# Kernel tuning notes

Hardware: AMD Instinct MI355X
Metric: run time of the kernel (lower is better)

The kernel has to match this reference:

```python
import jax, jax.numpy as jnp
import numpy as np

K = 7          # kernel_size (odd)
STRIDE = 1
PAD = K // 2
SIGMA_GUIDE = 1.0


def _unfold6(x, k, stride, pad):
    """torch F.unfold equivalent -> (bs, ch, k, k, oh, ow)."""
    bs, ch = x.shape[:2]
    patches = jax.lax.conv_general_dilated_patches(
        x, filter_shape=(k, k), window_strides=(stride, stride),
        padding=[(pad, pad), (pad, pad)])  # (bs, ch*k*k, oh, ow), channel-major
    oh, ow = patches.shape[2:]
    return patches.reshape(bs, ch, k, k, oh, ow)


def setup_inputs() -> dict:
    key = jax.random.key(0)
    k1, k2 = jax.random.split(key, 2)
    input = jax.random.normal(k1, (2, 32, 256, 256), dtype=jnp.float32)
    input_for_kernel = jax.random.normal(k2, (2, 3, 256, 256), dtype=jnp.float32)
    sigma_for_kernel = jnp.asarray(float(K) / 4.0, dtype=jnp.float32)  # Parameter init
    return {"input": input, "input_for_kernel": input_for_kernel,
            "sigma_for_kernel": sigma_for_kernel}


def reference(input, input_for_kernel, sigma_for_kernel):
    dt = input.dtype
    # spatial Gaussian kernel (truncated, normalized)
    r = jnp.arange(-(K // 2), K // 2 + 1, dtype=dt)
    g1 = jnp.exp(-0.5 * r * r / (sigma_for_kernel * sigma_for_kernel))
    g2 = g1[:, None] * g1[None, :]
    g2 = g2 / g2.sum()  # (K, K)

    # data-dependent range (guide) kernel: GaussKernel2dFn, channel_wise=False
    g = input_for_kernel / SIGMA_GUIDE                      # (b, cg, H, W)
    cols_g = _unfold6(g, K, STRIDE, PAD)                    # (b, cg, K, K, H, W)
    diff = cols_g - g[:, :, None, None]                     # center = window middle (stride 1)
    guide = jnp.exp(-0.5 * jnp.sum(diff * diff, axis=1, keepdims=True))  # (b,1,K,K,H,W)

    ker = g2[None, None, :, :, None, None] * guide          # (b,1,K,K,H,W)
    norm = ker.sum(axis=(2, 3), keepdims=True)
    ker = ker / (norm + (norm == 0).astype(dt))

    # ApplyKernelFn: unfold input, multiply by per-pixel kernel, sum over window
    in_cols = _unfold6(input, K, STRIDE, PAD)               # (b, c, K, K, H, W)
    out = jnp.einsum('bcklhw,bzklhw->bchw', in_cols, ker)
    return out
```

## Files before the change

### kernel.cpp

```cpp
#include <hip/hip_runtime.h>

#define KS    7
#define RAD   3
#define TW    32
#define TH    8
#define HR    14
#define PAIRS 21
#define NSITE (HR*2*PAIRS)
#define H     256
#define W     256
#define HWp   (H*W)
#define NTASK2 (HR*10*2)

typedef __fp16    h2raw __attribute__((ext_vector_type(2)));
typedef _Float16  f16x2 __attribute__((ext_vector_type(2)));

__device__ __forceinline__ unsigned pk(float a, float b) {
    h2raw h = __builtin_amdgcn_cvt_pkrtz(a, b);
    return __builtin_bit_cast(unsigned, h);
}
__device__ __forceinline__ f16x2 bch(unsigned u) {
    return __builtin_bit_cast(f16x2, u);
}

#if __has_builtin(__builtin_amdgcn_fdot2)
__device__ __forceinline__ float fdot2(f16x2 a, f16x2 b, float c) {
    return __builtin_amdgcn_fdot2(a, b, c, false);
}
#else
__device__ __forceinline__ float fdot2(f16x2 a, f16x2 b, float c) {
    return c + (float)a.x * (float)b.x + (float)a.y * (float)b.y;
}
#endif

#if __has_builtin(__builtin_amdgcn_exp2f)
__device__ __forceinline__ float fexp2(float x) { return __builtin_amdgcn_exp2f(x); }
#else
__device__ __forceinline__ float fexp2(float x) { return exp2f(x); }
#endif

__device__ __forceinline__ void pkfma(f16x2& d, f16x2 a, f16x2 b) {
    asm("v_pk_fma_f16 %0, %1, %2, %0" : "+v"(d) : "v"(a), "v"(b));
}

#define BAR() asm volatile("s_waitcnt lgkmcnt(0)\n\ts_barrier" ::: "memory")

#define ISSUE_IN(g) do {                                                    \
    _Pragma("unroll")                                                       \
    for (int j = 0; j < 2; ++j) {                                           \
        iA[j] = make_float4(0.f, 0.f, 0.f, 0.f);                            \
        iB[j] = iA[j]; iC[j] = iA[j]; iD[j] = iA[j];                        \
        if (tv[j]) {                                                        \
            const float* p = inb + (size_t)((g) * 8 + 4 * tcpp[j]) * HWp    \
                             + toff[j];                                     \
            iA[j] = *(const float4*)p;                                      \
            iB[j] = *(const float4*)(p + HWp);                              \
            iC[j] = *(const float4*)(p + 2 * HWp);                          \
            iD[j] = *(const float4*)(p + 3 * HWp);                          \
        }                                                                   \
    }                                                                       \
} while (0)

#define WRITE_IN(g) do {                                                    \
    _Pragma("unroll")                                                       \
    for (int j = 0; j < 2; ++j) {                                           \
        if (tok[j]) {                                                       \
            unsigned* bp = &dtu[(g)][ts0[j] * 4 + tcpp[j] * 2];             \
            *(uint2*)bp = make_uint2(pk(iA[j].y, iB[j].y),                  \
                                     pk(iC[j].y, iD[j].y));                 \
            *(uint2*)(bp + PAIRS * 4) = make_uint2(pk(iA[j].z, iB[j].z),    \
                                                   pk(iC[j].z, iD[j].z));   \
            if (!tq0[j])                                                    \
                *(uint2*)(bp + (PAIRS - 1) * 4) =                           \
                    make_uint2(pk(iA[j].x, iB[j].x), pk(iC[j].x, iD[j].x)); \
            if (!tq9[j])                                                    \
                *(uint2*)(bp + 4) =                                         \
                    make_uint2(pk(iA[j].w, iB[j].w), pk(iC[j].w, iD[j].w)); \
        }                                                                   \
    }                                                                       \
} while (0)

#define APPLY(g) do {                                                       \
    const uint4* dg = (const uint4*)&dtu[(g)][0];                           \
    float acc[8];                                                           \
    _Pragma("unroll") for (int c = 0; c < 8; ++c) acc[c] = 0.f;             \
    f16x2 A0 = (f16x2)0, A1 = (f16x2)0, A2 = (f16x2)0, A3 = (f16x2)0;       \
    _Pragma("unroll")                                                       \
    for (int i = 0; i < KS; ++i) {                                          \
        const int rb = (ty + i) * 2 * PAIRS;                                \
        uint4 rq[KS];                                                       \
        _Pragma("unroll")                                                   \
        for (int k = 0; k < KS; ++k) rq[k] = dg[rb + colAdd[k]];            \
        _Pragma("unroll")                                                   \
        for (int k = 0; k < KS; ++k) {                                      \
            f16x2 wh = bch(wkp[i * KS + k]);                                \
            pkfma(A0, wh, bch(rq[k].x));                                    \
            pkfma(A1, wh, bch(rq[k].y));                                    \
            pkfma(A2, wh, bch(rq[k].z));                                    \
            pkfma(A3, wh, bch(rq[k].w));                                    \
        }                                                                   \
        if (i == 3) {         \
            acc[0] += (float)A0.x; acc[1] += (float)A0.y;                   \
            acc[2] += (float)A1.x; acc[3] += (float)A1.y;                   \
            acc[4] += (float)A2.x; acc[5] += (float)A2.y;                   \
            acc[6] += (float)A3.x; acc[7] += (float)A3.y;                   \
            A0 = (f16x2)0; A1 = (f16x2)0; A2 = (f16x2)0; A3 = (f16x2)0;     \
        }                                                                   \
    }                                                                       \
    acc[0] += (float)A0.x; acc[1] += (float)A0.y;                           \
    acc[2] += (float)A1.x; acc[3] += (float)A1.y;                           \
    acc[4] += (float)A2.x; acc[5] += (float)A2.y;                           \
    acc[6] += (float)A3.x; acc[7] += (float)A3.y;                           \
    float* ob = out + ((size_t)b * 32 + (g) * 8) * HWp                      \
                + (size_t)Yo * W + Xo;                                      \
    _Pragma("unroll")                                                       \
    for (int c = 0; c < 8; ++c) ob[(size_t)c * HWp] = acc[c] * inv;         \
} while (0)

__global__ __launch_bounds__(256)
void bilateral_kernel(const float* __restrict__ in,
                      const float* __restrict__ guide,
                      const float* __restrict__ sigma_p,
                      float* __restrict__ out)
{
    __shared__ uint2 gt2[NSITE];
    __shared__ __align__(16) unsigned dtu[4][NSITE * 4];

    const int tid = threadIdx.x;
    const int tx  = tid & 31;
    const int ty  = tid >> 5;
    const int x0  = blockIdx.x * TW;
    const int y0  = blockIdx.y * TH;
    const int b   = blockIdx.z;

    const float* gb  = guide + (size_t)b * 3  * HWp;
    const float* inb = in    + (size_t)b * 32 * HWp;

    const float sigma = sigma_p[0];
    const float isig2 = 1.0f / (sigma * sigma);
    const float L2E   = 1.442695041f;
    const float SQL   = 1.201122409f;
    float lnT2[KS];
#pragma unroll
    for (int i = 0; i < KS; ++i) {
        float r = (float)(i - RAD);
        lnT2[i] = -0.5f * r * r * isig2 * L2E;
    }

    bool tok[2], tv[2], tq0[2], tq9[2];
    int  tcpp[2], toff[2], ts0[2];
#pragma unroll
    for (int j = 0; j < 2; ++j) {
        int t = tid + j * 256;
        tok[j] = t < NTASK2;
        int row = t / 20;
        int rem = t - row * 20;
        int q   = rem >> 1;
        tcpp[j] = rem & 1;
        int gy  = y0 - RAD + row;
        int gxb = x0 - 4 + 4 * q;
        tv[j]   = tok[j] && gy >= 0 && gy < H && gxb >= 0 && gxb < W;
        toff[j] = gy * W + gxb;
        ts0[j]  = row * 2 * PAIRS + 2 * q;
        tq0[j]  = (q == 0);
        tq9[j]  = (q == 9);
    }

    float4 gX = make_float4(0.f, 0.f, 0.f, 0.f), gY = gX, gZ = gX;
    int grow = 0, gq = 0;
    if (tid < HR * 10) {
        grow = tid / 10; gq = tid - grow * 10;
        int gy  = y0 - RAD + grow;
        int gxb = x0 - 4 + 4 * gq;
        if (gy >= 0 && gy < H && gxb >= 0 && gxb < W) {
            const float* p = gb + gy * W + gxb;
            gX = *(const float4*)p;
            gY = *(const float4*)(p + HWp);
            gZ = *(const float4*)(p + 2 * HWp);
        }
    }
    float4 iA[2], iB[2], iC[2], iD[2];
    ISSUE_IN(0);

    if (tid < HR * 10) {
        int s0 = grow * 2 * PAIRS + 2 * gq;
        const float xs[4] = {gX.x, gX.y, gX.z, gX.w};
        const float ys[4] = {gY.x, gY.y, gY.z, gY.w};
        const float zs[4] = {gZ.x, gZ.y, gZ.z, gZ.w};
        const int   st[4] = {s0 + PAIRS - 1, s0, s0 + PAIRS, s0 + 1};
#pragma unroll
        for (int j = 0; j < 4; ++j) {
            if ((gq == 0 && j == 0) || (gq == 9 && j == 3)) continue;
            float ax = xs[j] * SQL, ay = ys[j] * SQL, az = zs[j] * SQL;
            float qv = -0.5f * (ax * ax + ay * ay + az * az);
            gt2[st[j]] = make_uint2(pk(ax, ay), pk(az, qv));
        }
    }
    BAR();

    int colAdd[KS];
#pragma unroll
    for (int k = 0; k < KS; ++k) {
        int col = tx + k;
        colAdd[k] = (col & 1) * PAIRS + (col >> 1);
    }

    const int ccol = tx + RAD;
    uint2 cr = gt2[(ty + RAD) * 2 * PAIRS + (ccol & 1) * PAIRS + (ccol >> 1)];
    const f16x2 cxy = bch(cr.x);
    f16x2 czq = bch(cr.y);
    const float qc = (float)czq.y;
    f16x2 cz1;
    cz1.x = czq.x; cz1.y = (_Float16)1.0f;

    unsigned wkp[KS * KS];
    float nsum = 0.f;
#pragma unroll
    for (int i = 0; i < KS; ++i) {
        const int rb = (ty + i) * 2 * PAIRS;
        const float Qi = lnT2[i] + qc;
#pragma unroll
        for (int k = 0; k < KS; ++k) {
            uint2 g = gt2[rb + colAdd[k]];
            float e = fdot2(bch(g.x), cxy, fdot2(bch(g.y), cz1, Qi + lnT2[k]));
            float w = fexp2(e);
            nsum += w;
            wkp[i * KS + k] = pk(w, w);
        }
    }
    const float inv = 1.f / nsum;
    const int Xo = x0 + tx, Yo = y0 + ty;

    WRITE_IN(0);
    ISSUE_IN(1);
    BAR();
    APPLY(0);
    WRITE_IN(1);
    ISSUE_IN(2);
    BAR();
    APPLY(1);
    WRITE_IN(2);
    ISSUE_IN(3);
    BAR();
    APPLY(2);
    WRITE_IN(3);
    BAR();
    APPLY(3);
}

extern "C" void kernel_launch(void* const* d_in, const int* in_sizes, int n_in,
                              void* d_out, int out_size, void* d_ws, size_t ws_size,
                              hipStream_t stream) {
    const float* in    = (const float*)d_in[0];
    const float* guide = (const float*)d_in[1];
    const float* sigma = (const float*)d_in[2];
    float* out = (float*)d_out;
    dim3 grid(W / TW, H / TH, 2);
    bilateral_kernel<<<grid, dim3(256), 0, stream>>>(in, guide, sigma, out);
}
```

Baseline: 19.63 us.

## Compute two adjacent output pixels per thread and double tile height

Each thread now handles two horizontally adjacent pixels, so TH grows to 16 with 16 threads per row. The packed f16 weights hold both pixels' weights, and op_sel on v_pk_fma_f16 selects the lo or hi weight. Eight LDS column loads now feed both pixels' 7 taps, which cuts LDS reads per output, and results are stored as float2. The cost is twice the accumulator registers and a larger shared halo per block (HR 22), which may lower occupancy. The other shared-loading code is not shown, so it is unclear whether its task counts were updated to match the new tile height.

```diff
diff --git a/kernel.cpp b/kernel.cpp
--- a/kernel.cpp
+++ b/kernel.cpp
@@ -3,8 +3,8 @@
 #define KS    7
 #define RAD   3
 #define TW    32
-#define TH    8
-#define HR    14
+#define TH    16
+#define HR    22
 #define PAIRS 21
 #define NSITE (HR*2*PAIRS)
 #define H     256
@@ -39,8 +39,13 @@
 __device__ __forceinline__ float fexp2(float x) { return exp2f(x); }
 #endif
 
-__device__ __forceinline__ void pkfma(f16x2& d, f16x2 a, f16x2 b) {
-    asm("v_pk_fma_f16 %0, %1, %2, %0" : "+v"(d) : "v"(a), "v"(b));
+__device__ __forceinline__ void pkfma_lo(f16x2& d, f16x2 w, f16x2 x) {
+    asm("v_pk_fma_f16 %0, %1, %2, %0 op_sel:[0,0,0] op_sel_hi:[0,1,1]"
+        : "+v"(d) : "v"(w), "v"(x));
+}
+__device__ __forceinline__ void pkfma_hi(f16x2& d, f16x2 w, f16x2 x) {
+    asm("v_pk_fma_f16 %0, %1, %2, %0 op_sel:[1,0,0] op_sel_hi:[1,1,1]"
+        : "+v"(d) : "v"(w), "v"(x));
 }
 
 #define BAR() asm volatile("s_waitcnt lgkmcnt(0)\n\ts_barrier" ::: "memory")
@@ -82,39 +87,58 @@
 
 #define APPLY(g) do {                                                       \
     const uint4* dg = (const uint4*)&dtu[(g)][0];                           \
-    float acc[8];                                                           \
-    _Pragma("unroll") for (int c = 0; c < 8; ++c) acc[c] = 0.f;             \
+    float acc0[8], acc1[8];                                                 \
+    _Pragma("unroll") for (int c = 0; c < 8; ++c) { acc0[c] = 0.f; acc1[c] = 0.f; } \
     f16x2 A0 = (f16x2)0, A1 = (f16x2)0, A2 = (f16x2)0, A3 = (f16x2)0;       \
+    f16x2 B0 = (f16x2)0, B1 = (f16x2)0, B2 = (f16x2)0, B3 = (f16x2)0;       \
     _Pragma("unroll")                                                       \
     for (int i = 0; i < KS; ++i) {                                          \
         const int rb = (ty + i) * 2 * PAIRS;                                \
-        uint4 rq[KS];                                                       \
+        uint4 rq[8];                                                        \
         _Pragma("unroll")                                                   \
-        for (int k = 0; k < KS; ++k) rq[k] = dg[rb + colAdd[k]];            \
+        for (int m = 0; m < 8; ++m) rq[m] = dg[rb + colAdd8[m]];            \
         _Pragma("unroll")                                                   \
         for (int k = 0; k < KS; ++k) {                                      \
             f16x2 wh = bch(wkp[i * KS + k]);                                \
-            pkfma(A0, wh, bch(rq[k].x));                                    \
-            pkfma(A1, wh, bch(rq[k].y));                                    \
-            pkfma(A2, wh, bch(rq[k].z));                                    \
-            pkfma(A3, wh, bch(rq[k].w));                                    \
+            pkfma_lo(A0, wh, bch(rq[k].x));                                 \
+            pkfma_lo(A1, wh, bch(rq[k].y));                                 \
+            pkfma_lo(A2, wh, bch(rq[k].z));                                 \
+            pkfma_lo(A3, wh, bch(rq[k].w));                                 \
+            pkfma_hi(B0, wh, bch(rq[k + 1].x));                             \
+            pkfma_hi(B1, wh, bch(rq[k + 1].y));                             \
+            pkfma_hi(B2, wh, bch(rq[k + 1].z));                             \
+            pkfma_hi(B3, wh, bch(rq[k + 1].w));                             \
         }                                                                   \
         if (i == 3) {         \
-            acc[0] += (float)A0.x; acc[1] += (float)A0.y;                   \
-            acc[2] += (float)A1.x; acc[3] += (float)A1.y;                   \
-            acc[4] += (float)A2.x; acc[5] += (float)A2.y;                   \
-            acc[6] += (float)A3.x; acc[7] += (float)A3.y;                   \
+            acc0[0] += (float)A0.x; acc0[1] += (float)A0.y;                 \
+            acc0[2] += (float)A1.x; acc0[3] += (float)A1.y;                 \
+            acc0[4] += (float)A2.x; acc0[5] += (float)A2.y;                 \
+            acc0[6] += (float)A3.x; acc0[7] += (float)A3.y;                 \
+            acc1[0] += (float)B0.x; acc1[1] += (float)B0.y;                 \
+            acc1[2] += (float)B1.x; acc1[3] += (float)B1.y;                 \
+            acc1[4] += (float)B2.x; acc1[5] += (float)B2.y;                 \
+            acc1[6] += (float)B3.x; acc1[7] += (float)B3.y;                 \
             A0 = (f16x2)0; A1 = (f16x2)0; A2 = (f16x2)0; A3 = (f16x2)0;     \
-        }                                                                   \
-    }                                                                       \
-    acc[0] += (float)A0.x; acc[1] += (float)A0.y;                           \
-    acc[2] += (float)A1.x; acc[3] += (float)A1.y;                           \
-    acc[4] += (float)A2.x; acc[5] += (float)A2.y;                           \
-    acc[6] += (float)A3.x; acc[7] += (float)A3.y;                           \
+            B0 = (f16x2)0; B1 = (f16x2)0; B2 = (f16x2)0; B3 = (f16x2)0;     \
+        }                                                                   \
+    }                                                                       \
+    acc0[0] += (float)A0.x; acc0[1] += (float)A0.y;                         \
+    acc0[2] += (float)A1.x; acc0[3] += (float)A1.y;                         \
+    acc0[4] += (float)A2.x; acc0[5] += (float)A2.y;                         \
+    acc0[6] += (float)A3.x; acc0[7] += (float)A3.y;                         \
+    acc1[0] += (float)B0.x; acc1[1] += (float)B0.y;                         \
+    acc1[2] += (float)B1.x; acc1[3] += (float)B1.y;                         \
+    acc1[4] += (float)B2.x; acc1[5] += (float)B2.y;                         \
+    acc1[6] += (float)B3.x; acc1[7] += (float)B3.y;                         \
     float* ob = out + ((size_t)b * 32 + (g) * 8) * HWp                      \
                 + (size_t)Yo * W + Xo;                                      \
     _Pragma("unroll")                                                       \
-    for (int c = 0; c < 8; ++c) ob[(size_t)c * HWp] = acc[c] * inv;         \
+    for (int c = 0; c < 8; ++c) {                                           \
+        float2 s;                                                           \
+        s.x = acc0[c] * inv0;                                               \
+        s.y = acc1[c] * inv1;                                               \
+        *(float2*)(ob + (size_t)c * HWp) = s;                               \
+    }                                                                       \
 } while (0)
 
 __global__ __launch_bounds__(256)
@@ -127,8 +151,8 @@
     __shared__ __align__(16) unsigned dtu[4][NSITE * 4];
 
     const int tid = threadIdx.x;
-    const int tx  = tid & 31;
-    const int ty  = tid >> 5;
+    const int tx  = tid & 15;
+    const int ty  = tid >> 4;
     const int x0  = blockIdx.x * TW;
     const int y0  = blockIdx.y * TH;
     const int b   = blockIdx.z;
@@ -198,38 +222,46 @@
     }
     BAR();
 
-    int colAdd[KS];
-#pragma unroll
-    for (int k = 0; k < KS; ++k) {
-        int col = tx + k;
-        colAdd[k] = (col & 1) * PAIRS + (col >> 1);
-    }
-
-    const int ccol = tx + RAD;
-    uint2 cr = gt2[(ty + RAD) * 2 * PAIRS + (ccol & 1) * PAIRS + (ccol >> 1)];
-    const f16x2 cxy = bch(cr.x);
-    f16x2 czq = bch(cr.y);
-    const float qc = (float)czq.y;
-    f16x2 cz1;
-    cz1.x = czq.x; cz1.y = (_Float16)1.0f;
+    int colAdd8[8];
+#pragma unroll
+    for (int m = 0; m < 8; ++m)
+        colAdd8[m] = (m & 1) * PAIRS + tx + (m >> 1);
+
+    const int cb = (ty + RAD) * 2 * PAIRS;
+    uint2 c0r = gt2[cb + colAdd8[3]];
+    uint2 c1r = gt2[cb + colAdd8[4]];
+    const f16x2 cxy0 = bch(c0r.x), cxy1 = bch(c1r.x);
+    f16x2 czq0 = bch(c0r.y), czq1 = bch(c1r.y);
+    const float qc0 = (float)czq0.y, qc1 = (float)czq1.y;
+    f16x2 cz10, cz11;
+    cz10.x = czq0.x; cz10.y = (_Float16)1.0f;
+    cz11.x = czq1.x; cz11.y = (_Float16)1.0f;
 
     unsigned wkp[KS * KS];
-    float nsum = 0.f;
+    float ns0 = 0.f, ns1 = 0.f;
 #pragma unroll
     for (int i = 0; i < KS; ++i) {
         const int rb = (ty + i) * 2 * PAIRS;
-        const float Qi = lnT2[i] + qc;
+        uint2 gq2[8];
+#pragma unroll
+        for (int m = 0; m < 8; ++m) gq2[m] = gt2[rb + colAdd8[m]];
+        const float Qi0 = lnT2[i] + qc0;
+        const float Qi1 = lnT2[i] + qc1;
 #pragma unroll
         for (int k = 0; k < KS; ++k) {
-            uint2 g = gt2[rb + colAdd[k]];
-            float e = fdot2(bch(g.x), cxy, fdot2(bch(g.y), cz1, Qi + lnT2[k]));
-            float w = fexp2(e);
-            nsum += w;
-            wkp[i * KS + k] = pk(w, w);
+            float e0 = fdot2(bch(gq2[k].x), cxy0,
+                             fdot2(bch(gq2[k].y), cz10, Qi0 + lnT2[k]));
+            float w0 = fexp2(e0);
+            ns0 += w0;
+            float e1 = fdot2(bch(gq2[k + 1].x), cxy1,
+                             fdot2(bch(gq2[k + 1].y), cz11, Qi1 + lnT2[k]));
+            float w1 = fexp2(e1);
+            ns1 += w1;
+            wkp[i * KS + k] = pk(w0, w1);
         }
     }
-    const float inv = 1.f / nsum;
-    const int Xo = x0 + tx, Yo = y0 + ty;
+    const float inv0 = 1.f / ns0, inv1 = 1.f / ns1;
+    const int Xo = x0 + 2 * tx, Yo = y0 + ty;
 
     WRITE_IN(0);
     ISSUE_IN(1);
```

New measurement: 20.12 us. 1.02x slower.
